# Performance work log

Hardware: AMD Instinct MI355X
Metric: run time of the kernel (lower is better)

## Reference

```python
import jax, jax.numpy as jnp
import numpy as np

B, T, V, E, H, TAGS = 64, 512, 30000, 128, 256, 50


def setup_inputs() -> dict:
    key = jax.random.key(0)
    ks = jax.random.split(key, 24)

    def w(k, shape, scale=0.05):
        return jax.random.normal(k, shape, dtype=jnp.float32) * scale

    inp = {
        "words": jax.random.randint(ks[0], (B, T), 0, V),
        "lengths": jax.random.randint(ks[1], (B,), 0, T),
        "emb": w(ks[2], (V, E)),
    }
    i = 3
    for name, din in [("l1f", E), ("l1b", E), ("l2f", 2 * H), ("l2b", 2 * H)]:
        inp[name + "_Wih"] = w(ks[i], (4 * H, din))
        inp[name + "_Whh"] = w(ks[i + 1], (4 * H, H))
        inp[name + "_bih"] = w(ks[i + 2], (4 * H,))
        inp[name + "_bhh"] = w(ks[i + 3], (4 * H,))
        i += 4
    inp["cls_W"] = w(ks[i], (TAGS, 2 * H))
    inp["cls_b"] = w(ks[i + 1], (TAGS,))
    return inp


def lstm_dir(x, mask, Wih, Whh, bih, bhh, reverse):
    """Masked LSTMCell recurrence. x: [B,T,D], mask: [B,T] float. Returns [B,T,H]."""
    Bq = x.shape[0]
    Hh = Whh.shape[1]
    # Precompute input contribution for all timesteps: [B,T,4H]
    xg = jnp.einsum('btd,gd->btg', x, Wih) + bih

    def step(carry, inp):
        h, c = carry
        g_x, m = inp  # g_x: [B,4H], m: [B]
        gates = g_x + h @ Whh.T + bhh
        i_g, f_g, g_g, o_g = jnp.split(gates, 4, axis=-1)  # PyTorch gate order i,f,g,o
        c_new = jax.nn.sigmoid(f_g) * c + jax.nn.sigmoid(i_g) * jnp.tanh(g_g)
        h_new = jax.nn.sigmoid(o_g) * jnp.tanh(c_new)
        m = m[:, None]
        h = h_new * m + h * (1 - m)
        c = c_new * m + c * (1 - m)
        return (h, c), h

    init = (jnp.zeros((Bq, Hh), x.dtype), jnp.zeros((Bq, Hh), x.dtype))
    _, hs = jax.lax.scan(step, init, (xg.transpose(1, 0, 2), mask.T), reverse=reverse)
    return hs.transpose(1, 0, 2)


def bilstm(x, mask, fW, fU, fb1, fb2, bW, bU, bb1, bb2):
    fwd = lstm_dir(x, mask, fW, fU, fb1, fb2, reverse=False)
    bwd = lstm_dir(x, mask, bW, bU, bb1, bb2, reverse=True)
    return jnp.concatenate([fwd, bwd], axis=-1)


def reference(words, lengths, emb,
              l1f_Wih, l1f_Whh, l1f_bih, l1f_bhh,
              l1b_Wih, l1b_Whh, l1b_bih, l1b_bhh,
              l2f_Wih, l2f_Whh, l2f_bih, l2f_bhh,
              l2b_Wih, l2b_Whh, l2b_bih, l2b_bhh,
              cls_W, cls_b):
    mask = (lengths[:, None] > jnp.arange(T)).astype(jnp.float32)  # [B,T]
    x = emb[words]  # [B,T,E]
    o1 = bilstm(x, mask, l1f_Wih, l1f_Whh, l1f_bih, l1f_bhh,
                l1b_Wih, l1b_Whh, l1b_bih, l1b_bhh)  # [B,T,2H]
    o2 = bilstm(o1, mask, l2f_Wih, l2f_Whh, l2f_bih, l2f_bhh,
                l2b_Wih, l2b_Whh, l2b_bih, l2b_bhh)  # [B,T,2H]
    logits = jnp.einsum('bth,kh->btk', o2, cls_W) + cls_b  # [B,T,TAGS]
    return logits
```

## Files before the change

kernel.cpp:

```cpp
#include <hip/hip_runtime.h>
#include <hip/hip_bf16.h>

#define Bq 64
#define Tq 512
#define Eq 128
#define Hq 256
#define NTAGS 50
#define Mq (Bq*Tq)

typedef _Float16 v8hf __attribute__((ext_vector_type(8)));
typedef float v4f __attribute__((ext_vector_type(4)));

__device__ __forceinline__ float sigmoidf_(float x) { return 1.f / (1.f + __expf(-x)); }
__device__ __forceinline__ float tanhf_(float x) {
    float e = __expf(2.f * x);
    return 1.f - 2.f / (e + 1.f);
}

__global__ void detect_int64(const unsigned* __restrict__ words,
                             const unsigned* __restrict__ lens,
                             unsigned* __restrict__ dflags) {
    __shared__ int wbad, lbad, wnz, lnz;
    if (threadIdx.x == 0) { wbad = 0; lbad = 0; wnz = 0; lnz = 0; }
    __syncthreads();
    for (int i = threadIdx.x; i < 16384; i += blockDim.x) {
        if (words[2 * i + 1] != 0u) wbad = 1;
        if (words[2 * i] != 0u) wnz = 1;
    }
    for (int i = threadIdx.x; i < 32; i += blockDim.x) {
        if (lens[2 * i + 1] != 0u) lbad = 1;
        if (lens[2 * i] != 0u) lnz = 1;
    }
    __syncthreads();
    if (threadIdx.x == 0) {
        unsigned f = 0;
        if (!wbad && wnz) f |= 1u;
        if (!lbad && lnz) f |= 2u;
        dflags[0] = f;
    }
}

__global__ void bias_kernel(const float* b1f_ih, const float* b1f_hh,
                            const float* b1b_ih, const float* b1b_hh,
                            const float* b2f_ih, const float* b2f_hh,
                            const float* b2b_ih, const float* b2b_hh,
                            float* bias) {
    int i = blockIdx.x * blockDim.x + threadIdx.x;
    if (i >= 4096) return;
    int l = i >> 11, d = (i >> 10) & 1, nn = i & 1023;
    float v;
    if (l == 0) v = d ? (b1b_ih[nn] + b1b_hh[nn]) : (b1f_ih[nn] + b1f_hh[nn]);
    else        v = d ? (b2b_ih[nn] + b2b_hh[nn]) : (b2f_ih[nn] + b2f_hh[nn]);
    bias[i] = v;
}

__global__ void pack_whh_mfma(const float* __restrict__ W, _Float16* __restrict__ PA) {
    int t = blockIdx.x * 256 + threadIdx.x;
    if (t >= 32768) return;
    int fg = t >> 6, lane = t & 63;
    int w = fg >> 5, rem = fg & 31, mtl = rem >> 3, kc = rem & 7;
    int grow = (w * 4 + mtl) * 16 + (lane & 15);
    int kb = kc * 32 + (lane >> 4) * 8;
    _Float16 h8[8];
    #pragma unroll
    for (int i = 0; i < 8; ++i) h8[i] = (_Float16)W[(size_t)grow * 256 + kb + i];
    *(uint4*)(PA + ((size_t)fg * 64 + lane) * 8) = *(const uint4*)h8;
}

__global__ void pack_w_bfrag(const float* __restrict__ W, _Float16* __restrict__ PB,
                             int Nvalid, int K, int nchunks) {
    int t = blockIdx.x * 256 + threadIdx.x;
    if (t >= nchunks) return;
    int fg = t >> 6, lane = t & 63;
    int kcn = K >> 5;
    int ntile = fg / kcn, kc = fg % kcn;
    int n = ntile * 16 + (lane & 15);
    int kb = kc * 32 + (lane >> 4) * 8;
    _Float16 h8[8];
    #pragma unroll
    for (int i = 0; i < 8; ++i)
        h8[i] = (n < Nvalid) ? (_Float16)W[(size_t)n * K + kb + i] : (_Float16)0.f;
    *(uint4*)(PB + ((size_t)fg * 64 + lane) * 8) = *(const uint4*)h8;
}

template<int AMODE, int OUTT>
__global__ __launch_bounds__(256)
void gemm_mfma(const _Float16* __restrict__ Asrc, const unsigned* __restrict__ words_u32,
               const float* __restrict__ emb, const unsigned* __restrict__ dflags,
               const _Float16* __restrict__ PB, const float* __restrict__ bias,
               void* __restrict__ Cptr, int Nstr, int K, int Nvalid)
{
    __shared__ _Float16 At[64 * 40];
    const int tid = threadIdx.x;
    const int w = tid >> 6, lane = tid & 63;
    const int n0w = blockIdx.x * 256 + w * 64;
    const int m0 = blockIdx.y * 64;
    const int srow = tid >> 2, sseg = tid & 3;
    const int kcn = K >> 5;
    const int ntb = n0w >> 4;
    bool w64 = false;
    if (AMODE == 2) w64 = (dflags[0] & 1u) != 0u;

    v4f acc[4][4] = {};
    for (int kc0 = 0; kc0 < kcn; ++kc0) {
        if (AMODE == 0) {
            uint4 v = *(const uint4*)(Asrc + (size_t)(m0 + srow) * K + kc0 * 32 + sseg * 8);
            *(uint4*)(At + srow * 40 + sseg * 8) = v;
        } else {
            int wd = (int)(w64 ? words_u32[2 * (m0 + srow)] : words_u32[m0 + srow]);
            const float* src = emb + (size_t)wd * Eq + kc0 * 32 + sseg * 8;
            float4 v0 = *(const float4*)src;
            float4 v1 = *(const float4*)(src + 4);
            _Float16 h8[8] = {(_Float16)v0.x, (_Float16)v0.y, (_Float16)v0.z, (_Float16)v0.w,
                              (_Float16)v1.x, (_Float16)v1.y, (_Float16)v1.z, (_Float16)v1.w};
            *(uint4*)(At + srow * 40 + sseg * 8) = *(const uint4*)h8;
        }
        __syncthreads();
        v8hf Bf[4];
        #pragma unroll
        for (int nf = 0; nf < 4; ++nf) {
            size_t fg = (size_t)(ntb + nf) * kcn + kc0;
            Bf[nf] = __builtin_bit_cast(v8hf, *(const uint4*)(PB + (fg * 64 + lane) * 8));
        }
        #pragma unroll
        for (int mf = 0; mf < 4; ++mf) {
            v8hf Af = __builtin_bit_cast(v8hf,
                *(const uint4*)(At + (mf * 16 + (lane & 15)) * 40 + (lane >> 4) * 8));
            #pragma unroll
            for (int nf = 0; nf < 4; ++nf)
                acc[mf][nf] = __builtin_amdgcn_mfma_f32_16x16x32_f16(Af, Bf[nf], acc[mf][nf], 0, 0, 0);
        }
        __syncthreads();
    }
    #pragma unroll
    for (int nf = 0; nf < 4; ++nf) {
        int colb = n0w + nf * 16 + (lane & 15);
        float bb = (colb < Nvalid) ? bias[colb] : 0.f;
        #pragma unroll
        for (int mf = 0; mf < 4; ++mf) {
            int rowb = m0 + mf * 16 + (lane >> 4) * 4;
            #pragma unroll
            for (int r = 0; r < 4; ++r) {
                float v = acc[mf][nf][r] + bb;
                if (OUTT == 1) {
                    ((_Float16*)Cptr)[(size_t)(rowb + r) * Nstr + colb] = (_Float16)v;
                } else {
                    if (colb < Nvalid)
                        ((float*)Cptr)[(size_t)(rowb + r) * Nstr + colb] = v;
                }
            }
        }
    }
}

__global__ __launch_bounds__(1024)
void lstm_mfma(const _Float16* __restrict__ xg,
               const _Float16* __restrict__ PAf, const _Float16* __restrict__ PAb,
               const unsigned* __restrict__ len_u32,
               const unsigned* __restrict__ dflags,
               _Float16* __restrict__ out)
{
    extern __shared__ char lds_raw[];
    _Float16* ldsA = (_Float16*)lds_raw;
    float*    gbuf = (float*)(lds_raw + 131072);
    _Float16* h16  = (_Float16*)(lds_raw + 131072 + 16512);

    const int tid = threadIdx.x;
    const int bid = blockIdx.x;
    const int dir = bid >> 4;
    const int b0  = (bid & 15) * 4;
    const int w    = tid >> 6;
    const int lane = tid & 63;
    const int n    = lane & 15;
    const int kg   = lane >> 4;
    const int bu   = tid >> 8;
    const int j    = tid & 255;
    const _Float16* __restrict__ PA = dir ? PAb : PAf;
    const bool l64 = (dflags[0] & 2u) != 0u;
    const int mylen = (int)(l64 ? len_u32[2 * (b0 + bu)] : len_u32[b0 + bu]);

    for (int chunk = tid; chunk < 8192; chunk += 1024) {
        int lfrag = chunk >> 6, lane_s = chunk & 63;
        int w_s = lfrag >> 3, kc_s = lfrag & 7;
        int fg = w_s * 32 + 8 + kc_s;
        *(uint4*)(ldsA + (size_t)chunk * 8) = *(const uint4*)(PA + ((size_t)fg * 64 + lane_s) * 8);
    }
    uint4 Ar[4];
    #pragma unroll
    for (int kc = 0; kc < 4; ++kc)
        Ar[kc] = *(const uint4*)(PA + ((size_t)(w * 32 + kc) * 64 + lane) * 8);

    float c = 0.f, hreg = 0.f;
    h16[0 * 1056 + bu * 264 + j] = (_Float16)0.f;
    __syncthreads();

    for (int t = 0; t < Tq; ++t) {
        const int teff = dir ? (Tq - 1 - t) : t;
        const int par = t & 1;
        const _Float16* hrd = h16 + par * 1056;

        const _Float16* xr = xg + ((size_t)(b0 + bu) * Tq + teff) * 2048 + dir * 1024 + j;
        float xv0 = (float)xr[0], xv1 = (float)xr[256], xv2 = (float)xr[512], xv3 = (float)xr[768];

        v4f acc0 = {0.f, 0.f, 0.f, 0.f};
        v4f acc1 = {0.f, 0.f, 0.f, 0.f};
        v4f acc2 = {0.f, 0.f, 0.f, 0.f};
        v4f acc3 = {0.f, 0.f, 0.f, 0.f};
        #pragma unroll
        for (int kc = 0; kc < 8; ++kc) {
            v8hf B;
            if (n < 4) {
                uint4 hb = *(const uint4*)(hrd + n * 264 + kc * 32 + kg * 8);
                B = __builtin_bit_cast(v8hf, hb);
            } else {
                uint4 z = {0u, 0u, 0u, 0u};
                B = __builtin_bit_cast(v8hf, z);
            }
            v8hf A0;
            if (kc < 4) A0 = __builtin_bit_cast(v8hf, Ar[kc]);
            else A0 = __builtin_bit_cast(v8hf, *(const uint4*)(PA + ((size_t)(w * 32 + kc) * 64 + lane) * 8));
            acc0 = __builtin_amdgcn_mfma_f32_16x16x32_f16(A0, B, acc0, 0, 0, 0);
            v8hf A1 = __builtin_bit_cast(v8hf, *(const uint4*)(ldsA + ((size_t)(w * 8 + kc) * 64 + lane) * 8));
            acc1 = __builtin_amdgcn_mfma_f32_16x16x32_f16(A1, B, acc1, 0, 0, 0);
            v8hf A2 = __builtin_bit_cast(v8hf, *(const uint4*)(PA + ((size_t)(w * 32 + 16 + kc) * 64 + lane) * 8));
            acc2 = __builtin_amdgcn_mfma_f32_16x16x32_f16(A2, B, acc2, 0, 0, 0);
            v8hf A3 = __builtin_bit_cast(v8hf, *(const uint4*)(PA + ((size_t)(w * 32 + 24 + kc) * 64 + lane) * 8));
            acc3 = __builtin_amdgcn_mfma_f32_16x16x32_f16(A3, B, acc3, 0, 0, 0);
        }
        if (n < 4) {
            float* gp = gbuf + n * 1032 + w * 64 + kg * 4;
            gp[0]  = acc0[0]; gp[1]  = acc0[1]; gp[2]  = acc0[2]; gp[3]  = acc0[3];
            gp[16] = acc1[0]; gp[17] = acc1[1]; gp[18] = acc1[2]; gp[19] = acc1[3];
            gp[32] = acc2[0]; gp[33] = acc2[1]; gp[34] = acc2[2]; gp[35] = acc2[3];
            gp[48] = acc3[0]; gp[49] = acc3[1]; gp[50] = acc3[2]; gp[51] = acc3[3];
        }
        __syncthreads();
        {
            float g0 = xv0 + gbuf[bu * 1032 + 0 * 256 + j];
            float g1 = xv1 + gbuf[bu * 1032 + 1 * 256 + j];
            float g2 = xv2 + gbuf[bu * 1032 + 2 * 256 + j];
            float g3 = xv3 + gbuf[bu * 1032 + 3 * 256 + j];
            float ig = sigmoidf_(g0), fg = sigmoidf_(g1);
            float gg = tanhf_(g2), og = sigmoidf_(g3);
            float cn = fg * c + ig * gg;
            float hn = og * tanhf_(cn);
            bool m = (teff < mylen);
            float hm = m ? hn : hreg;
            c = m ? cn : c;
            hreg = hm;
            h16[(par ^ 1) * 1056 + bu * 264 + j] = (_Float16)hm;
            size_t orow = (size_t)(b0 + bu) * Tq + teff;
            out[orow * 512 + dir * 256 + j] = (_Float16)hm;
        }
        __syncthreads();
    }
}

extern "C" void kernel_launch(void* const* d_in, const int* in_sizes, int n_in,
                              void* d_out, int out_size, void* d_ws, size_t ws_size,
                              hipStream_t stream)
{
    const unsigned* words  = (const unsigned*)d_in[0];
    const unsigned* lens   = (const unsigned*)d_in[1];
    const float* emb     = (const float*)d_in[2];
    const float* l1f_Wih = (const float*)d_in[3];
    const float* l1f_Whh = (const float*)d_in[4];
    const float* l1f_bih = (const float*)d_in[5];
    const float* l1f_bhh = (const float*)d_in[6];
    const float* l1b_Wih = (const float*)d_in[7];
    const float* l1b_Whh = (const float*)d_in[8];
    const float* l1b_bih = (const float*)d_in[9];
    const float* l1b_bhh = (const float*)d_in[10];
    const float* l2f_Wih = (const float*)d_in[11];
    const float* l2f_Whh = (const float*)d_in[12];
    const float* l2f_bih = (const float*)d_in[13];
    const float* l2f_bhh = (const float*)d_in[14];
    const float* l2b_Wih = (const float*)d_in[15];
    const float* l2b_Whh = (const float*)d_in[16];
    const float* l2b_bih = (const float*)d_in[17];
    const float* l2b_bhh = (const float*)d_in[18];
    const float* cls_W   = (const float*)d_in[19];
    const float* cls_b   = (const float*)d_in[20];
    (void)in_sizes; (void)n_in; (void)out_size; (void)ws_size;

    char* ws = (char*)d_ws;
    size_t off = 0;
    auto alloc = [&](size_t b) { void* p = ws + off; off += (b + 255) & ~(size_t)255; return p; };
    _Float16*  xg = (_Float16*)alloc((size_t)Mq * 2048 * 2);
    _Float16*  o1 = (_Float16*)alloc((size_t)Mq * 512 * 2);
    _Float16*  o2 = (_Float16*)alloc((size_t)Mq * 512 * 2);
    _Float16* PAk = (_Float16*)alloc((size_t)4 * 262144 * 2);
    _Float16* PB1 = (_Float16*)alloc((size_t)2 * 131072 * 2);
    _Float16* PB2 = (_Float16*)alloc((size_t)2 * 524288 * 2);
    _Float16* PBc = (_Float16*)alloc((size_t)131072 * 2);
    float* biasbuf = (float*)alloc((size_t)4 * 1024 * 4);
    unsigned* dflags = (unsigned*)alloc(256);

    _Float16* PA1f = PAk;
    _Float16* PA1b = PAk + 262144;
    _Float16* PA2f = PAk + 2 * 262144;
    _Float16* PA2b = PAk + 3 * 262144;

    const size_t ldsBytes = 131072 + 16512 + 4224;
    hipFuncSetAttribute((const void*)lstm_mfma, hipFuncAttributeMaxDynamicSharedMemorySize, (int)ldsBytes);

    detect_int64<<<1, 256, 0, stream>>>(words, lens, dflags);
    bias_kernel<<<dim3(16), 256, 0, stream>>>(l1f_bih, l1f_bhh, l1b_bih, l1b_bhh,
                                              l2f_bih, l2f_bhh, l2b_bih, l2b_bhh, biasbuf);
    pack_whh_mfma<<<dim3(128), 256, 0, stream>>>(l1f_Whh, PA1f);
    pack_whh_mfma<<<dim3(128), 256, 0, stream>>>(l1b_Whh, PA1b);
    pack_whh_mfma<<<dim3(128), 256, 0, stream>>>(l2f_Whh, PA2f);
    pack_whh_mfma<<<dim3(128), 256, 0, stream>>>(l2b_Whh, PA2b);
    pack_w_bfrag<<<dim3(64), 256, 0, stream>>>(l1f_Wih, PB1, 1024, 128, 16384);
    pack_w_bfrag<<<dim3(64), 256, 0, stream>>>(l1b_Wih, PB1 + 131072, 1024, 128, 16384);
    pack_w_bfrag<<<dim3(256), 256, 0, stream>>>(l2f_Wih, PB2, 1024, 512, 65536);
    pack_w_bfrag<<<dim3(256), 256, 0, stream>>>(l2b_Wih, PB2 + 524288, 1024, 512, 65536);
    pack_w_bfrag<<<dim3(64), 256, 0, stream>>>(cls_W, PBc, NTAGS, 512, 16384);

    gemm_mfma<2, 1><<<dim3(8, Mq / 64), 256, 0, stream>>>(nullptr, words, emb, dflags,
        PB1, biasbuf, xg, 2048, 128, 2048);
    lstm_mfma<<<32, 1024, ldsBytes, stream>>>(xg, PA1f, PA1b, lens, dflags, o1);
    gemm_mfma<0, 1><<<dim3(8, Mq / 64), 256, 0, stream>>>(o1, nullptr, nullptr, dflags,
        PB2, biasbuf + 2048, xg, 2048, 512, 2048);
    lstm_mfma<<<32, 1024, ldsBytes, stream>>>(xg, PA2f, PA2b, lens, dflags, o2);
    gemm_mfma<0, 0><<<dim3(1, Mq / 64), 256, 0, stream>>>(o2, nullptr, nullptr, dflags,
        PBc, cls_b, d_out, NTAGS, 512, NTAGS);
}
```

Baseline: 3.805 ms.

## Permute Whh packing so gate math runs in MFMA registers, dropping a barrier

Repacks the recurrent weight rows so each wave's four accumulators hold the i,f,g,o gates for the same hidden units. The LSTM cell update can then be computed directly from the MFMA accumulators in lanes n<4, which removes the LDS gate buffer and one __syncthreads per timestep. It also caches one more A-fragment per wave in LDS, and vectorizes the xg loads and h/out stores. The cost is that only 4 of 16 lanes per row group do the elementwise math, serializing the activations on fewer threads.

```diff
diff --git a/kernel.cpp b/kernel.cpp
--- a/kernel.cpp
+++ b/kernel.cpp
@@ -9,6 +9,7 @@
 #define Mq (Bq*Tq)
 
 typedef _Float16 v8hf __attribute__((ext_vector_type(8)));
+typedef _Float16 v4hf __attribute__((ext_vector_type(4)));
 typedef float v4f __attribute__((ext_vector_type(4)));
 
 __device__ __forceinline__ float sigmoidf_(float x) { return 1.f / (1.f + __expf(-x)); }
@@ -58,8 +59,8 @@
     int t = blockIdx.x * 256 + threadIdx.x;
     if (t >= 32768) return;
     int fg = t >> 6, lane = t & 63;
-    int w = fg >> 5, rem = fg & 31, mtl = rem >> 3, kc = rem & 7;
-    int grow = (w * 4 + mtl) * 16 + (lane & 15);
+    int w = fg >> 5, rem = fg & 31, g = rem >> 3, kc = rem & 7;
+    int grow = g * 256 + w * 16 + (lane & 15);
     int kb = kc * 32 + (lane >> 4) * 8;
     _Float16 h8[8];
     #pragma unroll
@@ -161,9 +162,9 @@
                _Float16* __restrict__ out)
 {
     extern __shared__ char lds_raw[];
-    _Float16* ldsA = (_Float16*)lds_raw;
-    float*    gbuf = (float*)(lds_raw + 131072);
-    _Float16* h16  = (_Float16*)(lds_raw + 131072 + 16512);
+    _Float16* ldsA  = (_Float16*)lds_raw;
+    _Float16* ldsA2 = (_Float16*)(lds_raw + 131072);
+    _Float16* h16   = (_Float16*)(lds_raw + 131072 + 16384);
 
     const int tid = threadIdx.x;
     const int bid = blockIdx.x;
@@ -173,11 +174,10 @@
     const int lane = tid & 63;
     const int n    = lane & 15;
     const int kg   = lane >> 4;
-    const int bu   = tid >> 8;
-    const int j    = tid & 255;
+    const int j0   = w * 16 + kg * 4;
     const _Float16* __restrict__ PA = dir ? PAb : PAf;
     const bool l64 = (dflags[0] & 2u) != 0u;
-    const int mylen = (int)(l64 ? len_u32[2 * (b0 + bu)] : len_u32[b0 + bu]);
+    const int mylen = (n < 4) ? (int)(l64 ? len_u32[2 * (b0 + n)] : len_u32[b0 + n]) : 0;
 
     for (int chunk = tid; chunk < 8192; chunk += 1024) {
         int lfrag = chunk >> 6, lane_s = chunk & 63;
@@ -185,22 +185,29 @@
         int fg = w_s * 32 + 8 + kc_s;
         *(uint4*)(ldsA + (size_t)chunk * 8) = *(const uint4*)(PA + ((size_t)fg * 64 + lane_s) * 8);
     }
+    {
+        int chunk = tid;
+        int w_s = chunk >> 6, lane_s = chunk & 63;
+        int fg = w_s * 32 + 16;
+        *(uint4*)(ldsA2 + (size_t)chunk * 8) = *(const uint4*)(PA + ((size_t)fg * 64 + lane_s) * 8);
+    }
     uint4 Ar[4];
     #pragma unroll
     for (int kc = 0; kc < 4; ++kc)
         Ar[kc] = *(const uint4*)(PA + ((size_t)(w * 32 + kc) * 64 + lane) * 8);
 
-    float c = 0.f, hreg = 0.f;
-    h16[0 * 1056 + bu * 264 + j] = (_Float16)0.f;
+    float c[4] = {0.f, 0.f, 0.f, 0.f};
+    float hreg[4] = {0.f, 0.f, 0.f, 0.f};
+    if (n < 4) {
+        v4hf z = {(_Float16)0.f, (_Float16)0.f, (_Float16)0.f, (_Float16)0.f};
+        *(uint2*)(h16 + 0 * 1056 + n * 264 + j0) = __builtin_bit_cast(uint2, z);
+    }
     __syncthreads();
 
     for (int t = 0; t < Tq; ++t) {
         const int teff = dir ? (Tq - 1 - t) : t;
         const int par = t & 1;
         const _Float16* hrd = h16 + par * 1056;
-
-        const _Float16* xr = xg + ((size_t)(b0 + bu) * Tq + teff) * 2048 + dir * 1024 + j;
-        float xv0 = (float)xr[0], xv1 = (float)xr[256], xv2 = (float)xr[512], xv3 = (float)xr[768];
 
         v4f acc0 = {0.f, 0.f, 0.f, 0.f};
         v4f acc1 = {0.f, 0.f, 0.f, 0.f};
@@ -222,35 +229,40 @@
             acc0 = __builtin_amdgcn_mfma_f32_16x16x32_f16(A0, B, acc0, 0, 0, 0);
             v8hf A1 = __builtin_bit_cast(v8hf, *(const uint4*)(ldsA + ((size_t)(w * 8 + kc) * 64 + lane) * 8));
             acc1 = __builtin_amdgcn_mfma_f32_16x16x32_f16(A1, B, acc1, 0, 0, 0);
-            v8hf A2 = __builtin_bit_cast(v8hf, *(const uint4*)(PA + ((size_t)(w * 32 + 16 + kc) * 64 + lane) * 8));
+            v8hf A2;
+            if (kc == 0) A2 = __builtin_bit_cast(v8hf, *(const uint4*)(ldsA2 + ((size_t)(w * 64 + lane)) * 8));
+            else A2 = __builtin_bit_cast(v8hf, *(const uint4*)(PA + ((size_t)(w * 32 + 16 + kc) * 64 + lane) * 8));
             acc2 = __builtin_amdgcn_mfma_f32_16x16x32_f16(A2, B, acc2, 0, 0, 0);
             v8hf A3 = __builtin_bit_cast(v8hf, *(const uint4*)(PA + ((size_t)(w * 32 + 24 + kc) * 64 + lane) * 8));
             acc3 = __builtin_amdgcn_mfma_f32_16x16x32_f16(A3, B, acc3, 0, 0, 0);
         }
         if (n < 4) {
-            float* gp = gbuf + n * 1032 + w * 64 + kg * 4;
-            gp[0]  = acc0[0]; gp[1]  = acc0[1]; gp[2]  = acc0[2]; gp[3]  = acc0[3];
-            gp[16] = acc1[0]; gp[17] = acc1[1]; gp[18] = acc1[2]; gp[19] = acc1[3];
-            gp[32] = acc2[0]; gp[33] = acc2[1]; gp[34] = acc2[2]; gp[35] = acc2[3];
-            gp[48] = acc3[0]; gp[49] = acc3[1]; gp[50] = acc3[2]; gp[51] = acc3[3];
-        }
-        __syncthreads();
-        {
-            float g0 = xv0 + gbuf[bu * 1032 + 0 * 256 + j];
-            float g1 = xv1 + gbuf[bu * 1032 + 1 * 256 + j];
-            float g2 = xv2 + gbuf[bu * 1032 + 2 * 256 + j];
-            float g3 = xv3 + gbuf[bu * 1032 + 3 * 256 + j];
-            float ig = sigmoidf_(g0), fg = sigmoidf_(g1);
-            float gg = tanhf_(g2), og = sigmoidf_(g3);
-            float cn = fg * c + ig * gg;
-            float hn = og * tanhf_(cn);
-            bool m = (teff < mylen);
-            float hm = m ? hn : hreg;
-            c = m ? cn : c;
-            hreg = hm;
-            h16[(par ^ 1) * 1056 + bu * 264 + j] = (_Float16)hm;
-            size_t orow = (size_t)(b0 + bu) * Tq + teff;
-            out[orow * 512 + dir * 256 + j] = (_Float16)hm;
+            const _Float16* xr = xg + ((size_t)(b0 + n) * Tq + teff) * 2048 + dir * 1024 + j0;
+            v4hf x0 = __builtin_bit_cast(v4hf, *(const uint2*)(xr));
+            v4hf x1 = __builtin_bit_cast(v4hf, *(const uint2*)(xr + 256));
+            v4hf x2 = __builtin_bit_cast(v4hf, *(const uint2*)(xr + 512));
+            v4hf x3 = __builtin_bit_cast(v4hf, *(const uint2*)(xr + 768));
+            const bool m = (teff < mylen);
+            v4hf hh4;
+            #pragma unroll
+            for (int r = 0; r < 4; ++r) {
+                float g0 = (float)x0[r] + acc0[r];
+                float g1 = (float)x1[r] + acc1[r];
+                float g2 = (float)x2[r] + acc2[r];
+                float g3 = (float)x3[r] + acc3[r];
+                float ig = sigmoidf_(g0), fg = sigmoidf_(g1);
+                float gg = tanhf_(g2), og = sigmoidf_(g3);
+                float cn = fg * c[r] + ig * gg;
+                float hn = og * tanhf_(cn);
+                float hm = m ? hn : hreg[r];
+                c[r] = m ? cn : c[r];
+                hreg[r] = hm;
+                hh4[r] = (_Float16)hm;
+            }
+            uint2 hw = __builtin_bit_cast(uint2, hh4);
+            *(uint2*)(h16 + (par ^ 1) * 1056 + n * 264 + j0) = hw;
+            size_t orow = (size_t)(b0 + n) * Tq + teff;
+            *(uint2*)(out + orow * 512 + dir * 256 + j0) = hw;
         }
         __syncthreads();
     }
@@ -301,7 +313,7 @@
     _Float16* PA2f = PAk + 2 * 262144;
     _Float16* PA2b = PAk + 3 * 262144;
 
-    const size_t ldsBytes = 131072 + 16512 + 4224;
+    const size_t ldsBytes = 131072 + 16384 + 4224;
     hipFuncSetAttribute((const void*)lstm_mfma, hipFuncAttributeMaxDynamicSharedMemorySize, (int)ldsBytes);
 
     detect_int64<<<1, 256, 0, stream>>>(words, lens, dflags);
```

Result: slower. 5.511 ms (+44.8%).
